# Kernel tuning notes

Hardware: AMD Instinct MI355X
Metric: run time of the kernel (lower is better)

## Reference

```python
import jax, jax.numpy as jnp
import numpy as np

B, S, D, H = 4, 1024, 1024, 16
DH = D // H  # head dim = 64
PAD = -1e7   # padding_num in source
EPS = 1e-3   # keras LayerNormalization default epsilon


def setup_inputs() -> dict:
    key = jax.random.key(0)
    ks = jax.random.split(key, 8)
    return {
        "queries": jax.random.normal(ks[0], (B, S, D), jnp.float32),
        "keys": jax.random.normal(ks[1], (B, S, D), jnp.float32),
        "values": jax.random.normal(ks[2], (B, S, D), jnp.float32),
        "query_masks": jax.random.randint(ks[3], (B, S), 0, 2, jnp.int32),
        "key_masks": jax.random.randint(ks[4], (B, S), 0, 2, jnp.int32),
        "Wq": jax.random.normal(ks[5], (D, D), jnp.float32) * (D ** -0.5),
        "Wk": jax.random.normal(ks[6], (D, D), jnp.float32) * (D ** -0.5),
        "Wv": jax.random.normal(ks[7], (D, D), jnp.float32) * (D ** -0.5),
        "gamma": jnp.ones((D,), jnp.float32),
        "beta": jnp.zeros((D,), jnp.float32),
    }


def reference(queries, keys, values, query_masks, key_masks, Wq, Wk, Wv, gamma, beta):
    # QKV projections (no bias)
    Q = queries @ Wq  # [B,S,D]
    K = keys @ Wk
    V = values @ Wv
    # split heads: tf.split(axis=2)+concat(axis=0) == head-major layout [H,B,S,DH]
    Qh = Q.reshape(B, S, H, DH).transpose(2, 0, 1, 3)
    Kh = K.reshape(B, S, H, DH).transpose(2, 0, 1, 3)
    Vh = V.reshape(B, S, H, DH).transpose(2, 0, 1, 3)
    # scaled scores; note source scales by head_dim ** 0.5 (d_k of split K)
    scores = jnp.einsum("hbqd,hbkd->hbqk", Qh, Kh) / (DH ** 0.5)
    # additive key mask: positions where key_mask==0 get large negative
    scores = jnp.where(key_masks[None, :, None, :] == 0, PAD, scores)
    attn = jax.nn.softmax(scores, axis=-1)
    # multiplicative query mask AFTER softmax (as in source)
    attn = attn * query_masks[None, :, :, None].astype(jnp.float32)
    out = jnp.einsum("hbqk,hbkd->hbqd", attn, Vh)  # [H,B,S,DH]
    # merge heads back: concat over feature axis in head order
    out = out.transpose(1, 2, 0, 3).reshape(B, S, D)
    # residual + LayerNorm
    res = queries + out
    mean = jnp.mean(res, axis=-1, keepdims=True)
    var = jnp.mean(jnp.square(res - mean), axis=-1, keepdims=True)
    return gamma * (res - mean) * jax.lax.rsqrt(var + EPS) + beta
```

## Files before the change

kernel.cpp:

```cpp
#include <hip/hip_runtime.h>

#define BB   4
#define SS   1024
#define DD   1024
#define HH   16
#define DHH  64
#define LN_EPS  (1e-3f)

typedef unsigned short u16;
typedef __attribute__((ext_vector_type(8))) short bf16x8;
typedef __attribute__((ext_vector_type(4))) float f32x4;

__device__ __forceinline__ u16 f2bf(float f) {
    union { float f; unsigned int u; } v; v.f = f;
    return (u16)((v.u + 0x7FFFu + ((v.u >> 16) & 1u)) >> 16);
}

__device__ __forceinline__ unsigned int cvt_pk_bf16(float lo, float hi) {
    unsigned int r;
    asm("v_cvt_pk_bf16_f32 %0, %1, %2" : "=v"(r) : "v"(lo), "v"(hi));
    return r;
}

__device__ __forceinline__ void cp16(void* lds, const void* g) {
    __builtin_amdgcn_global_load_lds(
        (const __attribute__((address_space(1))) unsigned int*)g,
        (__attribute__((address_space(3))) unsigned int*)lds, 16, 0, 0);
}

__global__ __launch_bounds__(256) void prep(const float* __restrict__ q,
                                            const float* __restrict__ k,
                                            const float* __restrict__ v,
                                            const float* __restrict__ Wq,
                                            const float* __restrict__ Wk,
                                            const float* __restrict__ Wv,
                                            u16* __restrict__ Abf,
                                            u16* __restrict__ WtA) {
    __shared__ float Ts[64][65];
    const int z = blockIdx.z;
    const int tid = threadIdx.x;
    if (z < 3) {
        const float* src = (z == 0) ? q : (z == 1) ? k : v;
        u16* dst = Abf + (size_t)z * ((size_t)BB * SS * DD);
        const int N8 = BB * SS * DD / 8;
        for (int i = blockIdx.x * 256 + tid; i < N8; i += 256 * 256) {
            const float4 f0 = ((const float4*)src)[i * 2];
            const float4 f1 = ((const float4*)src)[i * 2 + 1];
            union { u16 u[8]; uint4 o; } t;
            t.u[0] = f2bf(f0.x); t.u[1] = f2bf(f0.y);
            t.u[2] = f2bf(f0.z); t.u[3] = f2bf(f0.w);
            t.u[4] = f2bf(f1.x); t.u[5] = f2bf(f1.y);
            t.u[6] = f2bf(f1.z); t.u[7] = f2bf(f1.w);
            ((uint4*)dst)[i] = t.o;
        }
    } else {
        const float* W = (z == 3) ? Wq : (z == 4) ? Wk : Wv;
        u16* Wt = WtA + (size_t)(z - 3) * DD * DD;
        const int k0 = (blockIdx.x >> 4) * 64, n0 = (blockIdx.x & 15) * 64;
        #pragma unroll
        for (int it = 0; it < 4; ++it) {
            const int idx = tid + it * 256;
            const int r = idx >> 4, c4 = (idx & 15) * 4;
            const float4 vv = *(const float4*)&W[(size_t)(k0 + r) * DD + n0 + c4];
            Ts[r][c4 + 0] = vv.x; Ts[r][c4 + 1] = vv.y;
            Ts[r][c4 + 2] = vv.z; Ts[r][c4 + 3] = vv.w;
        }
        __syncthreads();
        const int n = tid >> 2, kc = (tid & 3) * 16;
        #pragma unroll
        for (int p = 0; p < 8; ++p) {
            const unsigned int lo = f2bf(Ts[kc + p * 2 + 0][n]);
            const unsigned int hi = f2bf(Ts[kc + p * 2 + 1][n]);
            *(unsigned int*)&Wt[(size_t)(n0 + n) * DD + k0 + kc + p * 2] = lo | (hi << 16);
        }
    }
}

__global__ __launch_bounds__(256, 3) void gemm_fused(const u16* __restrict__ Abf,
                                                     const u16* __restrict__ WtA,
                                                     u16* __restrict__ Qbf,
                                                     u16* __restrict__ Kbf,
                                                     u16* __restrict__ Vtb) {
    __shared__ u16 As[128 * 64];
    __shared__ u16 Bs[128 * 64];

    const int bid = blockIdx.x;
    const int swz = (bid & 7) * 96 + (bid >> 3);
    const int z   = swz >> 8;
    const int rem = swz & 255;
    const int m0  = (rem >> 3) * 128;
    const int n0  = (rem & 7) * 128;

    const u16* A  = Abf + (size_t)z * ((size_t)BB * SS * DD);
    const u16* Bm = WtA + (size_t)z * (DD * DD);

    const int tid  = threadIdx.x;
    const int wave = tid >> 6, lane = tid & 63;
    const int ln = lane & 15, quad = lane >> 4;
    const int mw = (wave & 1) * 64, nw = (wave >> 1) * 64;

    const int r0 = tid >> 3;
    const int c0 = (tid & 7) ^ (r0 & 7);
    const u16* srcA0 = A  + (size_t)(m0 + r0) * DD + c0 * 8;
    const u16* srcB0 = Bm + (size_t)(n0 + r0) * DD + c0 * 8;

    f32x4 acc[4][4] = {};

    for (int t = 0; t < 16; ++t) {
        const int koff = t * 64;
        __syncthreads();
        #pragma unroll
        for (int w = 0; w < 4; ++w) {
            cp16(&As[(w * 256 + wave * 64) * 8], srcA0 + (size_t)w * 32 * DD + koff);
            cp16(&Bs[(w * 256 + wave * 64) * 8], srcB0 + (size_t)w * 32 * DD + koff);
        }
        __syncthreads();

        #pragma unroll
        for (int kk = 0; kk < 2; ++kk) {
            bf16x8 af[4], bfv[4];
            #pragma unroll
            for (int i = 0; i < 4; ++i) {
                const int r = mw + i * 16 + ln;
                af[i] = *(const bf16x8*)&As[((r << 3) + ((kk * 4 + quad) ^ (r & 7))) << 3];
            }
            #pragma unroll
            for (int j = 0; j < 4; ++j) {
                const int r = nw + j * 16 + ln;
                bfv[j] = *(const bf16x8*)&Bs[((r << 3) + ((kk * 4 + quad) ^ (r & 7))) << 3];
            }
            __builtin_amdgcn_s_setprio(1);
            #pragma unroll
            for (int i = 0; i < 4; ++i)
                #pragma unroll
                for (int j = 0; j < 4; ++j)
                    acc[i][j] = __builtin_amdgcn_mfma_f32_16x16x32_bf16(af[i], bfv[j], acc[i][j], 0, 0, 0);
            __builtin_amdgcn_s_setprio(0);
        }
    }

    if (z < 2) {
        u16* C = (z == 0) ? Qbf : Kbf;
        const float scale = (z == 0) ? 0.18033688f : 1.0f;
        #pragma unroll
        for (int i = 0; i < 4; ++i) {
            const int mbase = m0 + mw + i * 16 + quad * 4;
            const int bb = mbase >> 10, sb = mbase & 1023;
            #pragma unroll
            for (int j = 0; j < 4; ++j) {
                const int n = n0 + nw + j * 16 + ln;
                const int hh = n >> 6, dh = n & 63;
                #pragma unroll
                for (int r = 0; r < 4; ++r)
                    C[(((size_t)bb * HH + hh) * SS + sb + r) * DHH + dh] =
                        f2bf(acc[i][j][r] * scale);
            }
        }
    } else {
        #pragma unroll
        for (int i = 0; i < 4; ++i) {
            const int mbase = m0 + mw + i * 16 + quad * 4;
            const int bb = mbase >> 10, sb = mbase & 1023;
            #pragma unroll
            for (int j = 0; j < 4; ++j) {
                const int n = n0 + nw + j * 16 + ln;
                const int hh = n >> 6, dh = n & 63;
                uint2 pk;
                pk.x = cvt_pk_bf16(acc[i][j][0], acc[i][j][1]);
                pk.y = cvt_pk_bf16(acc[i][j][2], acc[i][j][3]);
                *(uint2*)&Vtb[(((size_t)bb * HH + hh) * DHH + dh) * SS + sb] = pk;
            }
        }
    }
}

__global__ __launch_bounds__(512) void attn_mfma(const u16* __restrict__ Qg,
                                                 const u16* __restrict__ Kg,
                                                 const u16* __restrict__ Vtg,
                                                 const int* __restrict__ qmask,
                                                 const int* __restrict__ kmask,
                                                 float* __restrict__ O) {
    __shared__ u16 Ps[128 * 68];
    __shared__ u16 Ks[3][64 * 64];
    __shared__ u16 Vs[3][64 * 64];
    __shared__ float kmLds[SS];

    const int bid  = blockIdx.x;
    const int xcd  = bid & 7;
    const int rest = bid >> 3;
    const int bh   = (rest & 7) * 8 + xcd;
    const int qt   = rest >> 3;
    const int b    = bh >> 4, h = bh & 15;
    const int q0   = qt * 128;
    const int tid  = threadIdx.x;
    const int wave = tid >> 6, lane = tid & 63;
    const int ln = lane & 15, quad = lane >> 4;
    const size_t bhs = (size_t)b * HH + h;

    const int sr = tid >> 3, scsrc = (tid & 7) ^ ((tid >> 3) & 7);
    const u16* kSrc = &Kg[(bhs * SS + sr) * DHH + scsrc * 8];
    const u16* vSrc = &Vtg[(bhs * DHH + sr) * SS + scsrc * 8];
    auto stageKV = [&](int cb, int t) {
        cp16(&Ks[cb][wave * 512], kSrc + (size_t)t * 64 * DHH);
        cp16(&Vs[cb][wave * 512], vSrc + t * 64);
    };

    const u16* qrow = &Qg[(bhs * SS + q0 + wave * 16 + ln) * DHH];
    const bf16x8 qf0 = *(const bf16x8*)&qrow[quad * 8];
    const bf16x8 qf1 = *(const bf16x8*)&qrow[32 + quad * 8];
    asm volatile("" ::: "memory");
    if (wave < 4)
        cp16(&kmLds[wave * 256], &kmask[b * SS + (wave * 64 + lane) * 4]);
    stageKV(0, 0);
    stageKV(1, 1);
    asm volatile("s_waitcnt vmcnt(2)" ::: "memory");
    __builtin_amdgcn_s_barrier();

    {
        const int2 iv = *(const int2*)&kmLds[tid * 2];
        float2 fv; fv.x = (float)iv.x; fv.y = (float)iv.y;
        *(float2*)&kmLds[tid * 2] = fv;
    }
    asm volatile("s_waitcnt lgkmcnt(0)" ::: "memory");
    __builtin_amdgcn_s_barrier();

    int off[4][2];
    #pragma unroll
    for (int nt = 0; nt < 4; ++nt) {
        const int r = nt * 16 + ln;
        off[nt][0] = ((r << 3) + ((0 + quad) ^ (r & 7))) << 3;
        off[nt][1] = ((r << 3) + ((4 + quad) ^ (r & 7))) << 3;
    }

    f32x4 o[4] = {};
    float lsum = 0.f;
    const f32x4 zero = {0.f, 0.f, 0.f, 0.f};
    const int prow = (wave * 16 + ln) * 68;

    int cbC = 0, cbS = 2;
    for (int kt = 0; kt < SS / 64; ++kt) {
        if (kt + 2 < SS / 64) stageKV(cbS, kt + 2);

        const u16* Kc = Ks[cbC];
        const u16* Vc = Vs[cbC];

        #pragma unroll
        for (int nt = 0; nt < 4; ++nt) {
            const bf16x8 k0f = *(const bf16x8*)&Kc[off[nt][0]];
            const bf16x8 k1f = *(const bf16x8*)&Kc[off[nt][1]];
            f32x4 sacc = __builtin_amdgcn_mfma_f32_16x16x32_bf16(k0f, qf0, zero, 0, 0, 0);
            sacc = __builtin_amdgcn_mfma_f32_16x16x32_bf16(k1f, qf1, sacc, 0, 0, 0);
            const float4 fm = *(const float4*)&kmLds[kt * 64 + nt * 16 + quad * 4];
            const float p0 = fm.x * __builtin_amdgcn_exp2f(sacc[0]);
            const float p1 = fm.y * __builtin_amdgcn_exp2f(sacc[1]);
            const float p2 = fm.z * __builtin_amdgcn_exp2f(sacc[2]);
            const float p3 = fm.w * __builtin_amdgcn_exp2f(sacc[3]);
            lsum += (p0 + p1) + (p2 + p3);
            uint2 pk;
            pk.x = cvt_pk_bf16(p0, p1);
            pk.y = cvt_pk_bf16(p2, p3);
            *(uint2*)&Ps[prow + nt * 16 + quad * 4] = pk;
        }

        __builtin_amdgcn_s_setprio(1);
        #pragma unroll
        for (int kk2 = 0; kk2 < 2; ++kk2) {
            const bf16x8 pf = *(const bf16x8*)&Ps[prow + kk2 * 32 + quad * 8];
            #pragma unroll
            for (int nt2 = 0; nt2 < 4; ++nt2) {
                const bf16x8 vf = *(const bf16x8*)&Vc[off[nt2][kk2]];
                o[nt2] = __builtin_amdgcn_mfma_f32_16x16x32_bf16(pf, vf, o[nt2], 0, 0, 0);
            }
        }
        __builtin_amdgcn_s_setprio(0);

        if (kt < SS / 64 - 1) {
            if (kt + 2 < SS / 64) asm volatile("s_waitcnt vmcnt(2)" ::: "memory");
            else                  asm volatile("s_waitcnt vmcnt(0)" ::: "memory");
            __builtin_amdgcn_s_barrier();
        }
        cbC = (cbC == 2) ? 0 : cbC + 1;
        cbS = (cbS == 2) ? 0 : cbS + 1;
    }

    lsum += __shfl_xor(lsum, 16);
    lsum += __shfl_xor(lsum, 32);
    #pragma unroll
    for (int r = 0; r < 4; ++r) {
        const int qloc = quad * 4 + r;
        const float l = __shfl(lsum, qloc);
        const int q = q0 + wave * 16 + qloc;
        const float scale = (float)qmask[b * SS + q] / l;
        #pragma unroll
        for (int nt2 = 0; nt2 < 4; ++nt2)
            O[((size_t)b * SS + q) * DD + h * DHH + nt2 * 16 + ln] = o[nt2][r] * scale;
    }
}

__global__ __launch_bounds__(256) void ln_kernel(const float* __restrict__ Qin,
                                                 const float* __restrict__ attn,
                                                 const float* __restrict__ gamma,
                                                 const float* __restrict__ beta,
                                                 float* __restrict__ out) {
    const int tid = threadIdx.x;
    const int wid = tid >> 6, lane = tid & 63;
    const int row = blockIdx.x * 4 + wid;
    const float4* qp = (const float4*)Qin + (size_t)row * 256;
    const float4* ap = (const float4*)attn + (size_t)row * 256;

    float4 v[4];
    float sum = 0.f;
    #pragma unroll
    for (int i = 0; i < 4; ++i) {
        const float4 qv = qp[lane + 64 * i];
        const float4 av = ap[lane + 64 * i];
        float4 t;
        t.x = qv.x + av.x; t.y = qv.y + av.y;
        t.z = qv.z + av.z; t.w = qv.w + av.w;
        v[i] = t;
        sum += (t.x + t.y) + (t.z + t.w);
    }
    #pragma unroll
    for (int off = 1; off < 64; off <<= 1) sum += __shfl_xor(sum, off);
    const float mean = sum * (1.0f / DD);

    float vs = 0.f;
    #pragma unroll
    for (int i = 0; i < 4; ++i) {
        const float dx = v[i].x - mean, dy = v[i].y - mean;
        const float dz = v[i].z - mean, dw = v[i].w - mean;
        vs += (dx * dx + dy * dy) + (dz * dz + dw * dw);
    }
    #pragma unroll
    for (int off = 1; off < 64; off <<= 1) vs += __shfl_xor(vs, off);
    const float inv = rsqrtf(vs * (1.0f / DD) + LN_EPS);

    #pragma unroll
    for (int i = 0; i < 4; ++i) {
        const float4 g  = ((const float4*)gamma)[lane + 64 * i];
        const float4 bt = ((const float4*)beta)[lane + 64 * i];
        float4 ov;
        ov.x = g.x * (v[i].x - mean) * inv + bt.x;
        ov.y = g.y * (v[i].y - mean) * inv + bt.y;
        ov.z = g.z * (v[i].z - mean) * inv + bt.z;
        ov.w = g.w * (v[i].w - mean) * inv + bt.w;
        ((float4*)out)[(size_t)row * 256 + lane + 64 * i] = ov;
    }
}

extern "C" void kernel_launch(void* const* d_in, const int* in_sizes, int n_in,
                              void* d_out, int out_size, void* d_ws, size_t ws_size,
                              hipStream_t stream) {
    const float* queries = (const float*)d_in[0];
    const float* keys    = (const float*)d_in[1];
    const float* values  = (const float*)d_in[2];
    const int*   qmask   = (const int*)d_in[3];
    const int*   kmask   = (const int*)d_in[4];
    const float* Wq      = (const float*)d_in[5];
    const float* Wk      = (const float*)d_in[6];
    const float* Wv      = (const float*)d_in[7];
    const float* gamma   = (const float*)d_in[8];
    const float* beta    = (const float*)d_in[9];
    float* out = (float*)d_out;

    const size_t NTOK = (size_t)BB * SS;
    u16* Abf = (u16*)d_ws;
    float* Ob = (float*)d_ws;
    u16* Qbf = Abf + 3 * NTOK * DD;
    u16* Kbf = Qbf + NTOK * DD;
    u16* Vtb = Kbf + NTOK * DD;
    u16* WtA = Vtb + NTOK * DD;

    prep<<<dim3(256, 1, 6), 256, 0, stream>>>(queries, keys, values, Wq, Wk, Wv, Abf, WtA);

    gemm_fused<<<768, 256, 0, stream>>>(Abf, WtA, Qbf, Kbf, Vtb);

    attn_mfma<<<BB * HH * (SS / 128), 512, 0, stream>>>(Qbf, Kbf, Vtb, qmask, kmask, Ob);

    ln_kernel<<<BB * SS / 4, 256, 0, stream>>>(queries, Ob, gamma, beta, out);
}
```

Before: 182.7 us.

## Split attention key tile across wave pairs with 32-query register blocking

Each wave now handles 32 query rows (two 16-row sub-tiles) and half of each 64-key tile, so K and V fragments loaded from LDS are reused across two query sub-tiles. The two key halves produce partial O accumulators and row sums, which are reduced through LDS scratch (reusing the KV buffers) in an epilogue before normalization and store. Launch bounds add a minimum-blocks hint. The extra epilogue barrier, LDS traffic and doubled accumulator registers are the trade-off against fewer LDS fragment reads per MFMA.

Measured after the change: 184.8 us. About the same (+1.2%).

```diff
diff --git a/kernel.cpp b/kernel.cpp
--- a/kernel.cpp
+++ b/kernel.cpp
@@ -174,15 +174,14 @@
     }
 }
 
-__global__ __launch_bounds__(512) void attn_mfma(const u16* __restrict__ Qg,
-                                                 const u16* __restrict__ Kg,
-                                                 const u16* __restrict__ Vtg,
-                                                 const int* __restrict__ qmask,
-                                                 const int* __restrict__ kmask,
-                                                 float* __restrict__ O) {
+__global__ __launch_bounds__(512, 4) void attn_mfma(const u16* __restrict__ Qg,
+                                                    const u16* __restrict__ Kg,
+                                                    const u16* __restrict__ Vtg,
+                                                    const int* __restrict__ qmask,
+                                                    const int* __restrict__ kmask,
+                                                    float* __restrict__ O) {
     __shared__ u16 Ps[128 * 68];
-    __shared__ u16 Ks[3][64 * 64];
-    __shared__ u16 Vs[3][64 * 64];
+    __shared__ u16 KVs[3][2][64 * 64];
     __shared__ float kmLds[SS];
 
     const int bid  = blockIdx.x;
@@ -195,19 +194,24 @@
     const int tid  = threadIdx.x;
     const int wave = tid >> 6, lane = tid & 63;
     const int ln = lane & 15, quad = lane >> 4;
+    const int qs4 = wave & 3;
+    const int kh  = wave >> 2;
     const size_t bhs = (size_t)b * HH + h;
 
     const int sr = tid >> 3, scsrc = (tid & 7) ^ ((tid >> 3) & 7);
     const u16* kSrc = &Kg[(bhs * SS + sr) * DHH + scsrc * 8];
     const u16* vSrc = &Vtg[(bhs * DHH + sr) * SS + scsrc * 8];
     auto stageKV = [&](int cb, int t) {
-        cp16(&Ks[cb][wave * 512], kSrc + (size_t)t * 64 * DHH);
-        cp16(&Vs[cb][wave * 512], vSrc + t * 64);
+        cp16(&KVs[cb][0][wave * 512], kSrc + (size_t)t * 64 * DHH);
+        cp16(&KVs[cb][1][wave * 512], vSrc + t * 64);
     };
 
-    const u16* qrow = &Qg[(bhs * SS + q0 + wave * 16 + ln) * DHH];
-    const bf16x8 qf0 = *(const bf16x8*)&qrow[quad * 8];
-    const bf16x8 qf1 = *(const bf16x8*)&qrow[32 + quad * 8];
+    const u16* qr0 = &Qg[(bhs * SS + q0 + qs4 * 32 + ln) * DHH];
+    bf16x8 qf[2][2];
+    qf[0][0] = *(const bf16x8*)&qr0[quad * 8];
+    qf[0][1] = *(const bf16x8*)&qr0[32 + quad * 8];
+    qf[1][0] = *(const bf16x8*)&qr0[16 * DHH + quad * 8];
+    qf[1][1] = *(const bf16x8*)&qr0[16 * DHH + 32 + quad * 8];
     asm volatile("" ::: "memory");
     if (wave < 4)
         cp16(&kmLds[wave * 256], &kmask[b * SS + (wave * 64 + lane) * 4]);
@@ -224,76 +228,129 @@
     asm volatile("s_waitcnt lgkmcnt(0)" ::: "memory");
     __builtin_amdgcn_s_barrier();
 
-    int off[4][2];
-    #pragma unroll
-    for (int nt = 0; nt < 4; ++nt) {
-        const int r = nt * 16 + ln;
-        off[nt][0] = ((r << 3) + ((0 + quad) ^ (r & 7))) << 3;
-        off[nt][1] = ((r << 3) + ((4 + quad) ^ (r & 7))) << 3;
-    }
-
-    f32x4 o[4] = {};
-    float lsum = 0.f;
+    int offk[2][2], offv[4], pps[2], wps[2][2];
+    #pragma unroll
+    for (int nt = 0; nt < 2; ++nt) {
+        const int r = kh * 32 + nt * 16 + ln;
+        offk[nt][0] = ((r << 3) + ((0 + quad) ^ (r & 7))) << 3;
+        offk[nt][1] = ((r << 3) + ((4 + quad) ^ (r & 7))) << 3;
+    }
+    #pragma unroll
+    for (int nt2 = 0; nt2 < 4; ++nt2) {
+        const int r = nt2 * 16 + ln;
+        offv[nt2] = ((r << 3) + ((kh * 4 + quad) ^ (r & 7))) << 3;
+    }
+    #pragma unroll
+    for (int qs = 0; qs < 2; ++qs) {
+        pps[qs] = (qs4 * 32 + qs * 16 + ln) * 68 + kh * 32 + quad * 8;
+        wps[qs][0] = (qs4 * 32 + qs * 16 + ln) * 68 + kh * 32 + quad * 4;
+        wps[qs][1] = wps[qs][0] + 16;
+    }
+
+    f32x4 o[2][4] = {};
+    float lsum[2] = {0.f, 0.f};
     const f32x4 zero = {0.f, 0.f, 0.f, 0.f};
-    const int prow = (wave * 16 + ln) * 68;
+    const int NT = SS / 64;
 
     int cbC = 0, cbS = 2;
-    for (int kt = 0; kt < SS / 64; ++kt) {
-        if (kt + 2 < SS / 64) stageKV(cbS, kt + 2);
-
-        const u16* Kc = Ks[cbC];
-        const u16* Vc = Vs[cbC];
-
-        #pragma unroll
-        for (int nt = 0; nt < 4; ++nt) {
-            const bf16x8 k0f = *(const bf16x8*)&Kc[off[nt][0]];
-            const bf16x8 k1f = *(const bf16x8*)&Kc[off[nt][1]];
-            f32x4 sacc = __builtin_amdgcn_mfma_f32_16x16x32_bf16(k0f, qf0, zero, 0, 0, 0);
-            sacc = __builtin_amdgcn_mfma_f32_16x16x32_bf16(k1f, qf1, sacc, 0, 0, 0);
-            const float4 fm = *(const float4*)&kmLds[kt * 64 + nt * 16 + quad * 4];
-            const float p0 = fm.x * __builtin_amdgcn_exp2f(sacc[0]);
-            const float p1 = fm.y * __builtin_amdgcn_exp2f(sacc[1]);
-            const float p2 = fm.z * __builtin_amdgcn_exp2f(sacc[2]);
-            const float p3 = fm.w * __builtin_amdgcn_exp2f(sacc[3]);
-            lsum += (p0 + p1) + (p2 + p3);
-            uint2 pk;
-            pk.x = cvt_pk_bf16(p0, p1);
-            pk.y = cvt_pk_bf16(p2, p3);
-            *(uint2*)&Ps[prow + nt * 16 + quad * 4] = pk;
+    for (int kt = 0; kt < NT; ++kt) {
+        if (kt + 2 < NT) stageKV(cbS, kt + 2);
+
+        const u16* Kc = KVs[cbC][0];
+        const u16* Vc = KVs[cbC][1];
+
+        const bf16x8 kf00 = *(const bf16x8*)&Kc[offk[0][0]];
+        const bf16x8 kf01 = *(const bf16x8*)&Kc[offk[0][1]];
+        const bf16x8 kf10 = *(const bf16x8*)&Kc[offk[1][0]];
+        const bf16x8 kf11 = *(const bf16x8*)&Kc[offk[1][1]];
+        #pragma unroll
+        for (int qs = 0; qs < 2; ++qs) {
+            #pragma unroll
+            for (int nt = 0; nt < 2; ++nt) {
+                f32x4 sacc = __builtin_amdgcn_mfma_f32_16x16x32_bf16(
+                    nt ? kf10 : kf00, qf[qs][0], zero, 0, 0, 0);
+                sacc = __builtin_amdgcn_mfma_f32_16x16x32_bf16(
+                    nt ? kf11 : kf01, qf[qs][1], sacc, 0, 0, 0);
+                const float4 fm = *(const float4*)&kmLds[kt * 64 + kh * 32 + nt * 16 + quad * 4];
+                const float p0 = fm.x * __builtin_amdgcn_exp2f(sacc[0]);
+                const float p1 = fm.y * __builtin_amdgcn_exp2f(sacc[1]);
+                const float p2 = fm.z * __builtin_amdgcn_exp2f(sacc[2]);
+                const float p3 = fm.w * __builtin_amdgcn_exp2f(sacc[3]);
+                lsum[qs] += (p0 + p1) + (p2 + p3);
+                uint2 pk;
+                pk.x = cvt_pk_bf16(p0, p1);
+                pk.y = cvt_pk_bf16(p2, p3);
+                *(uint2*)&Ps[wps[qs][nt]] = pk;
+            }
         }
 
         __builtin_amdgcn_s_setprio(1);
-        #pragma unroll
-        for (int kk2 = 0; kk2 < 2; ++kk2) {
-            const bf16x8 pf = *(const bf16x8*)&Ps[prow + kk2 * 32 + quad * 8];
-            #pragma unroll
-            for (int nt2 = 0; nt2 < 4; ++nt2) {
-                const bf16x8 vf = *(const bf16x8*)&Vc[off[nt2][kk2]];
-                o[nt2] = __builtin_amdgcn_mfma_f32_16x16x32_bf16(pf, vf, o[nt2], 0, 0, 0);
-            }
+        const bf16x8 vf0 = *(const bf16x8*)&Vc[offv[0]];
+        const bf16x8 vf1 = *(const bf16x8*)&Vc[offv[1]];
+        const bf16x8 vf2 = *(const bf16x8*)&Vc[offv[2]];
+        const bf16x8 vf3 = *(const bf16x8*)&Vc[offv[3]];
+        #pragma unroll
+        for (int qs2 = 0; qs2 < 2; ++qs2) {
+            const bf16x8 pf = *(const bf16x8*)&Ps[pps[qs2]];
+            o[qs2][0] = __builtin_amdgcn_mfma_f32_16x16x32_bf16(pf, vf0, o[qs2][0], 0, 0, 0);
+            o[qs2][1] = __builtin_amdgcn_mfma_f32_16x16x32_bf16(pf, vf1, o[qs2][1], 0, 0, 0);
+            o[qs2][2] = __builtin_amdgcn_mfma_f32_16x16x32_bf16(pf, vf2, o[qs2][2], 0, 0, 0);
+            o[qs2][3] = __builtin_amdgcn_mfma_f32_16x16x32_bf16(pf, vf3, o[qs2][3], 0, 0, 0);
         }
         __builtin_amdgcn_s_setprio(0);
 
-        if (kt < SS / 64 - 1) {
-            if (kt + 2 < SS / 64) asm volatile("s_waitcnt vmcnt(2)" ::: "memory");
-            else                  asm volatile("s_waitcnt vmcnt(0)" ::: "memory");
+        if (kt < NT - 1) {
+            if (kt + 2 < NT) asm volatile("s_waitcnt vmcnt(2)" ::: "memory");
+            else             asm volatile("s_waitcnt vmcnt(0)" ::: "memory");
             __builtin_amdgcn_s_barrier();
         }
         cbC = (cbC == 2) ? 0 : cbC + 1;
         cbS = (cbS == 2) ? 0 : cbS + 1;
     }
 
-    lsum += __shfl_xor(lsum, 16);
-    lsum += __shfl_xor(lsum, 32);
-    #pragma unroll
-    for (int r = 0; r < 4; ++r) {
-        const int qloc = quad * 4 + r;
-        const float l = __shfl(lsum, qloc);
-        const int q = q0 + wave * 16 + qloc;
-        const float scale = (float)qmask[b * SS + q] / l;
-        #pragma unroll
-        for (int nt2 = 0; nt2 < 4; ++nt2)
-            O[((size_t)b * SS + q) * DD + h * DHH + nt2 * 16 + ln] = o[nt2][r] * scale;
+    #pragma unroll
+    for (int qs = 0; qs < 2; ++qs) {
+        lsum[qs] += __shfl_xor(lsum[qs], 16);
+        lsum[qs] += __shfl_xor(lsum[qs], 32);
+    }
+    asm volatile("s_waitcnt lgkmcnt(0) vmcnt(0)" ::: "memory");
+    __builtin_amdgcn_s_barrier();
+
+    float* Osc = (float*)KVs;
+    float* lsc = kmLds;
+    if (kh) {
+        #pragma unroll
+        for (int qs2 = 0; qs2 < 2; ++qs2) {
+            const int qq = qs4 * 32 + qs2 * 16 + quad * 4;
+            #pragma unroll
+            for (int nt2 = 0; nt2 < 4; ++nt2)
+                *(f32x4*)&Osc[(nt2 * 16 + ln) * 132 + qq] = o[qs2][nt2];
+            if (quad == 0) lsc[qs4 * 32 + qs2 * 16 + ln] = lsum[qs2];
+        }
+    }
+    asm volatile("s_waitcnt lgkmcnt(0)" ::: "memory");
+    __builtin_amdgcn_s_barrier();
+    if (!kh) {
+        #pragma unroll
+        for (int qs2 = 0; qs2 < 2; ++qs2) {
+            const float ltot = lsum[qs2] + lsc[qs4 * 32 + qs2 * 16 + ln];
+            const int qq = qs4 * 32 + qs2 * 16 + quad * 4;
+            f32x4 oo[4];
+            #pragma unroll
+            for (int nt2 = 0; nt2 < 4; ++nt2)
+                oo[nt2] = *(const f32x4*)&Osc[(nt2 * 16 + ln) * 132 + qq];
+            #pragma unroll
+            for (int r = 0; r < 4; ++r) {
+                const int qloc = quad * 4 + r;
+                const float l = __shfl(ltot, qloc);
+                const int q = q0 + qs4 * 32 + qs2 * 16 + qloc;
+                const float scale = (float)qmask[b * SS + q] / l;
+                #pragma unroll
+                for (int nt2 = 0; nt2 < 4; ++nt2)
+                    O[((size_t)b * SS + q) * DD + h * DHH + nt2 * 16 + ln] =
+                        (o[qs2][nt2][r] + oo[nt2][r]) * scale;
+            }
+        }
     }
 }
 
```

## Fuse fp32-to-bf16 activation conversion into projection GEMM; double-buffer attention K/V

Applied to the files above, without the earlier changes.

The separate prep pass that converted the fp32 q/k/v activations to bf16 in global memory is removed. The projection GEMM now stages fp32 tiles into LDS with a swizzle and converts them to bf16 in registers before each MFMA, which removes a full write and re-read of the activation tensors. The GEMM's A tile doubles in LDS size (32KB fp32), which may reduce occupancy, and it adds conversion ALU work and twice the global bytes per A tile. Attention drops from triple to double buffering of K/V, with an extra barrier per iteration before issuing the next prefetch.

Result: slower. 194.3 us (+6.4%).

```diff
diff --git a/kernel.cpp b/kernel.cpp
--- a/kernel.cpp
+++ b/kernel.cpp
@@ -28,61 +28,43 @@
         (__attribute__((address_space(3))) unsigned int*)lds, 16, 0, 0);
 }
 
-__global__ __launch_bounds__(256) void prep(const float* __restrict__ q,
-                                            const float* __restrict__ k,
-                                            const float* __restrict__ v,
-                                            const float* __restrict__ Wq,
+__global__ __launch_bounds__(256) void prep(const float* __restrict__ Wq,
                                             const float* __restrict__ Wk,
                                             const float* __restrict__ Wv,
-                                            u16* __restrict__ Abf,
                                             u16* __restrict__ WtA) {
     __shared__ float Ts[64][65];
     const int z = blockIdx.z;
     const int tid = threadIdx.x;
-    if (z < 3) {
-        const float* src = (z == 0) ? q : (z == 1) ? k : v;
-        u16* dst = Abf + (size_t)z * ((size_t)BB * SS * DD);
-        const int N8 = BB * SS * DD / 8;
-        for (int i = blockIdx.x * 256 + tid; i < N8; i += 256 * 256) {
-            const float4 f0 = ((const float4*)src)[i * 2];
-            const float4 f1 = ((const float4*)src)[i * 2 + 1];
-            union { u16 u[8]; uint4 o; } t;
-            t.u[0] = f2bf(f0.x); t.u[1] = f2bf(f0.y);
-            t.u[2] = f2bf(f0.z); t.u[3] = f2bf(f0.w);
-            t.u[4] = f2bf(f1.x); t.u[5] = f2bf(f1.y);
-            t.u[6] = f2bf(f1.z); t.u[7] = f2bf(f1.w);
-            ((uint4*)dst)[i] = t.o;
-        }
-    } else {
-        const float* W = (z == 3) ? Wq : (z == 4) ? Wk : Wv;
-        u16* Wt = WtA + (size_t)(z - 3) * DD * DD;
-        const int k0 = (blockIdx.x >> 4) * 64, n0 = (blockIdx.x & 15) * 64;
-        #pragma unroll
-        for (int it = 0; it < 4; ++it) {
-            const int idx = tid + it * 256;
-            const int r = idx >> 4, c4 = (idx & 15) * 4;
-            const float4 vv = *(const float4*)&W[(size_t)(k0 + r) * DD + n0 + c4];
-            Ts[r][c4 + 0] = vv.x; Ts[r][c4 + 1] = vv.y;
-            Ts[r][c4 + 2] = vv.z; Ts[r][c4 + 3] = vv.w;
-        }
-        __syncthreads();
-        const int n = tid >> 2, kc = (tid & 3) * 16;
-        #pragma unroll
-        for (int p = 0; p < 8; ++p) {
-            const unsigned int lo = f2bf(Ts[kc + p * 2 + 0][n]);
-            const unsigned int hi = f2bf(Ts[kc + p * 2 + 1][n]);
-            *(unsigned int*)&Wt[(size_t)(n0 + n) * DD + k0 + kc + p * 2] = lo | (hi << 16);
-        }
-    }
-}
-
-__global__ __launch_bounds__(256, 3) void gemm_fused(const u16* __restrict__ Abf,
+    const float* W = (z == 0) ? Wq : (z == 1) ? Wk : Wv;
+    u16* Wt = WtA + (size_t)z * DD * DD;
+    const int k0 = (blockIdx.x >> 4) * 64, n0 = (blockIdx.x & 15) * 64;
+    #pragma unroll
+    for (int it = 0; it < 4; ++it) {
+        const int idx = tid + it * 256;
+        const int r = idx >> 4, c4 = (idx & 15) * 4;
+        const float4 vv = *(const float4*)&W[(size_t)(k0 + r) * DD + n0 + c4];
+        Ts[r][c4 + 0] = vv.x; Ts[r][c4 + 1] = vv.y;
+        Ts[r][c4 + 2] = vv.z; Ts[r][c4 + 3] = vv.w;
+    }
+    __syncthreads();
+    const int n = tid >> 2, kc = (tid & 3) * 16;
+    #pragma unroll
+    for (int p = 0; p < 8; ++p) {
+        const unsigned int lo = f2bf(Ts[kc + p * 2 + 0][n]);
+        const unsigned int hi = f2bf(Ts[kc + p * 2 + 1][n]);
+        *(unsigned int*)&Wt[(size_t)(n0 + n) * DD + k0 + kc + p * 2] = lo | (hi << 16);
+    }
+}
+
+__global__ __launch_bounds__(256, 3) void gemm_fused(const float* __restrict__ Qin,
+                                                     const float* __restrict__ Kin,
+                                                     const float* __restrict__ Vin,
                                                      const u16* __restrict__ WtA,
                                                      u16* __restrict__ Qbf,
                                                      u16* __restrict__ Kbf,
                                                      u16* __restrict__ Vtb) {
-    __shared__ u16 As[128 * 64];
-    __shared__ u16 Bs[128 * 64];
+    __shared__ float Asf[128 * 64];
+    __shared__ u16  Bs[128 * 64];
 
     const int bid = blockIdx.x;
     const int swz = (bid & 7) * 96 + (bid >> 3);
@@ -91,18 +73,27 @@
     const int m0  = (rem >> 3) * 128;
     const int n0  = (rem & 7) * 128;
 
-    const u16* A  = Abf + (size_t)z * ((size_t)BB * SS * DD);
-    const u16* Bm = WtA + (size_t)z * (DD * DD);
+    const float* A32 = (z == 0) ? Qin : (z == 1) ? Kin : Vin;
+    const u16*   Bm  = WtA + (size_t)z * (DD * DD);
 
     const int tid  = threadIdx.x;
     const int wave = tid >> 6, lane = tid & 63;
     const int ln = lane & 15, quad = lane >> 4;
     const int mw = (wave & 1) * 64, nw = (wave >> 1) * 64;
 
+    const int rA = tid >> 4;
+    const int cA = (tid & 15) ^ rA;
+    const float* srcA0 = A32 + (size_t)(m0 + rA) * DD + cA * 4;
     const int r0 = tid >> 3;
     const int c0 = (tid & 7) ^ (r0 & 7);
-    const u16* srcA0 = A  + (size_t)(m0 + r0) * DD + c0 * 8;
     const u16* srcB0 = Bm + (size_t)(n0 + r0) * DD + c0 * 8;
+
+    int rbA[4], rbB[4];
+    #pragma unroll
+    for (int i = 0; i < 4; ++i) {
+        rbA[i] = (mw + i * 16 + ln) * 64;
+        rbB[i] = (nw + i * 16 + ln) << 3;
+    }
 
     f32x4 acc[4][4] = {};
 
@@ -110,10 +101,11 @@
         const int koff = t * 64;
         __syncthreads();
         #pragma unroll
-        for (int w = 0; w < 4; ++w) {
-            cp16(&As[(w * 256 + wave * 64) * 8], srcA0 + (size_t)w * 32 * DD + koff);
+        for (int s = 0; s < 8; ++s)
+            cp16(&Asf[(s * 256 + wave * 64) * 4], srcA0 + (size_t)s * 16 * DD + koff);
+        #pragma unroll
+        for (int w = 0; w < 4; ++w)
             cp16(&Bs[(w * 256 + wave * 64) * 8], srcB0 + (size_t)w * 32 * DD + koff);
-        }
         __syncthreads();
 
         #pragma unroll
@@ -121,13 +113,20 @@
             bf16x8 af[4], bfv[4];
             #pragma unroll
             for (int i = 0; i < 4; ++i) {
-                const int r = mw + i * 16 + ln;
-                af[i] = *(const bf16x8*)&As[((r << 3) + ((kk * 4 + quad) ^ (r & 7))) << 3];
+                const int c0f = (kk * 8 + quad * 2) ^ ln;
+                const f32x4 a0 = *(const f32x4*)&Asf[rbA[i] + c0f * 4];
+                const f32x4 a1 = *(const f32x4*)&Asf[rbA[i] + (c0f ^ 1) * 4];
+                union { uint4 u; bf16x8 b; } cv;
+                cv.u.x = cvt_pk_bf16(a0.x, a0.y);
+                cv.u.y = cvt_pk_bf16(a0.z, a0.w);
+                cv.u.z = cvt_pk_bf16(a1.x, a1.y);
+                cv.u.w = cvt_pk_bf16(a1.z, a1.w);
+                af[i] = cv.b;
             }
             #pragma unroll
             for (int j = 0; j < 4; ++j) {
                 const int r = nw + j * 16 + ln;
-                bfv[j] = *(const bf16x8*)&Bs[((r << 3) + ((kk * 4 + quad) ^ (r & 7))) << 3];
+                bfv[j] = *(const bf16x8*)&Bs[(rbB[j] + ((kk * 4 + quad) ^ (r & 7))) << 3];
             }
             __builtin_amdgcn_s_setprio(1);
             #pragma unroll
@@ -181,8 +180,8 @@
                                                  const int* __restrict__ kmask,
                                                  float* __restrict__ O) {
     __shared__ u16 Ps[128 * 68];
-    __shared__ u16 Ks[3][64 * 64];
-    __shared__ u16 Vs[3][64 * 64];
+    __shared__ u16 Ks[2][64 * 64];
+    __shared__ u16 Vs[2][64 * 64];
     __shared__ float kmLds[SS];
 
     const int bid  = blockIdx.x;
@@ -200,7 +199,8 @@
     const int sr = tid >> 3, scsrc = (tid & 7) ^ ((tid >> 3) & 7);
     const u16* kSrc = &Kg[(bhs * SS + sr) * DHH + scsrc * 8];
     const u16* vSrc = &Vtg[(bhs * DHH + sr) * SS + scsrc * 8];
-    auto stageKV = [&](int cb, int t) {
+    auto stageKV = [&](int t) {
+        const int cb = t & 1;
         cp16(&Ks[cb][wave * 512], kSrc + (size_t)t * 64 * DHH);
         cp16(&Vs[cb][wave * 512], vSrc + t * 64);
     };
@@ -211,8 +211,8 @@
     asm volatile("" ::: "memory");
     if (wave < 4)
         cp16(&kmLds[wave * 256], &kmask[b * SS + (wave * 64 + lane) * 4]);
-    stageKV(0, 0);
-    stageKV(1, 1);
+    stageKV(0);
+    stageKV(1);
     asm volatile("s_waitcnt vmcnt(2)" ::: "memory");
     __builtin_amdgcn_s_barrier();
 
@@ -237,12 +237,11 @@
     const f32x4 zero = {0.f, 0.f, 0.f, 0.f};
     const int prow = (wave * 16 + ln) * 68;
 
-    int cbC = 0, cbS = 2;
+    #pragma unroll 2
     for (int kt = 0; kt < SS / 64; ++kt) {
-        if (kt + 2 < SS / 64) stageKV(cbS, kt + 2);
-
-        const u16* Kc = Ks[cbC];
-        const u16* Vc = Vs[cbC];
+        const int cb = kt & 1;
+        const u16* Kc = Ks[cb];
+        const u16* Vc = Vs[cb];
 
         #pragma unroll
         for (int nt = 0; nt < 4; ++nt) {
@@ -274,13 +273,15 @@
         }
         __builtin_amdgcn_s_setprio(0);
 
-        if (kt < SS / 64 - 1) {
-            if (kt + 2 < SS / 64) asm volatile("s_waitcnt vmcnt(2)" ::: "memory");
-            else                  asm volatile("s_waitcnt vmcnt(0)" ::: "memory");
-            __builtin_amdgcn_s_barrier();
-        }
-        cbC = (cbC == 2) ? 0 : cbC + 1;
-        cbS = (cbS == 2) ? 0 : cbS + 1;
+        if (kt == SS / 64 - 1) break;
+        __builtin_amdgcn_s_barrier();
+        if (kt + 2 < SS / 64) {
+            stageKV(kt + 2);
+            asm volatile("s_waitcnt vmcnt(2)" ::: "memory");
+        } else {
+            asm volatile("s_waitcnt vmcnt(0)" ::: "memory");
+        }
+        __builtin_amdgcn_s_barrier();
     }
 
     lsum += __shfl_xor(lsum, 16);
@@ -364,16 +365,16 @@
     float* out = (float*)d_out;
 
     const size_t NTOK = (size_t)BB * SS;
-    u16* Abf = (u16*)d_ws;
+    u16* base = (u16*)d_ws;
     float* Ob = (float*)d_ws;
-    u16* Qbf = Abf + 3 * NTOK * DD;
+    u16* Qbf = base + 3 * NTOK * DD;
     u16* Kbf = Qbf + NTOK * DD;
     u16* Vtb = Kbf + NTOK * DD;
     u16* WtA = Vtb + NTOK * DD;
 
-    prep<<<dim3(256, 1, 6), 256, 0, stream>>>(queries, keys, values, Wq, Wk, Wv, Abf, WtA);
-
-    gemm_fused<<<768, 256, 0, stream>>>(Abf, WtA, Qbf, Kbf, Vtb);
+    prep<<<dim3(256, 1, 3), 256, 0, stream>>>(Wq, Wk, Wv, WtA);
+
+    gemm_fused<<<768, 256, 0, stream>>>(queries, keys, values, WtA, Qbf, Kbf, Vtb);
 
     attn_mfma<<<BB * HH * (SS / 128), 512, 0, stream>>>(Qbf, Kbf, Vtb, qmask, kmask, Ob);
 
```
